# Optimization experiments

Measured on AMD Instinct MI355X. Metric: run time of the kernel, lower is better.

Reference implementation:

```python
import jax, jax.numpy as jnp
import numpy as np

N = 100000
IN_CH = 128
HID = 128
H = HID // 2  # per-sign half width = 64
E = 1200000
L = 3  # num_layers


def _mean_agg(x, src, dst, n):
    # mean of x[src] scattered to dst (source_to_target message passing)
    s = jax.ops.segment_sum(x[src], dst, num_segments=n)
    cnt = jax.ops.segment_sum(jnp.ones(src.shape[0], x.dtype), dst, num_segments=n)
    return s / jnp.maximum(cnt, 1.0)[:, None]


def setup_inputs() -> dict:
    key = jax.random.key(0)
    ks = jax.random.split(key, 16)
    sc = 0.05
    inp = {
        "x": jax.random.normal(ks[0], (N, IN_CH), jnp.float32),
        "pos_edge_index": jax.random.randint(ks[1], (2, E), 0, N, jnp.int64),
        "neg_edge_index": jax.random.randint(ks[2], (2, E), 0, N, jnp.int64),
        # conv1 (first_aggr=True): per-sign Linear on aggregated + on root
        "Wp_l": jax.random.normal(ks[3], (IN_CH, H), jnp.float32) * sc,
        "Wp_r": jax.random.normal(ks[4], (IN_CH, H), jnp.float32) * sc,
        "bp": jnp.zeros((H,), jnp.float32),
        "Wn_l": jax.random.normal(ks[5], (IN_CH, H), jnp.float32) * sc,
        "Wn_r": jax.random.normal(ks[6], (IN_CH, H), jnp.float32) * sc,
        "bn": jnp.zeros((H,), jnp.float32),
        # convs (first_aggr=False), stacked over L-1 layers
        "Wl_pos": jax.random.normal(ks[7], (L - 1, 2 * H, H), jnp.float32) * sc,
        "Wr_pos": jax.random.normal(ks[8], (L - 1, H, H), jnp.float32) * sc,
        "b_pos": jnp.zeros((L - 1, H), jnp.float32),
        "Wl_neg": jax.random.normal(ks[9], (L - 1, 2 * H, H), jnp.float32) * sc,
        "Wr_neg": jax.random.normal(ks[10], (L - 1, H, H), jnp.float32) * sc,
        "b_neg": jnp.zeros((L - 1, H), jnp.float32),
    }
    return inp


def reference(x, pos_edge_index, neg_edge_index,
              Wp_l, Wp_r, bp, Wn_l, Wn_r, bn,
              Wl_pos, Wr_pos, b_pos, Wl_neg, Wr_neg, b_neg):
    n = x.shape[0]
    ps, pd = pos_edge_index[0], pos_edge_index[1]
    ns, nd = neg_edge_index[0], neg_edge_index[1]

    # ---- conv1, first_aggr=True ----
    agg_p = _mean_agg(x, ps, pd, n)   # [N, IN_CH]
    agg_n = _mean_agg(x, ns, nd, n)
    out_pos = agg_p @ Wp_l + x @ Wp_r + bp   # [N, H]
    out_neg = agg_n @ Wn_l + x @ Wn_r + bn
    z = jnp.tanh(jnp.concatenate([out_pos, out_neg], axis=1))  # [N, 2H]

    # ---- convs, first_aggr=False ----
    for l in range(Wl_pos.shape[0]):
        x_p, x_n = z[:, :H], z[:, H:]
        ap_p = _mean_agg(x_p, ps, pd, n)   # pos-agg of pos half
        an_n = _mean_agg(x_n, ns, nd, n)   # neg-agg of neg half
        ap_n = _mean_agg(x_n, ps, pd, n)   # pos-agg of neg half
        an_p = _mean_agg(x_p, ns, nd, n)   # neg-agg of pos half
        o_p = (jnp.concatenate([ap_p, an_n], axis=1) @ Wl_pos[l]
               + x_p @ Wr_pos[l] + b_pos[l])
        o_n = (jnp.concatenate([ap_n, an_p], axis=1) @ Wl_neg[l]
               + x_n @ Wr_neg[l] + b_neg[l])
        z = jnp.tanh(jnp.concatenate([o_p, o_n], axis=1))
    return z  # [N, HID]
```

## Files before the change

kernel.cpp:

```cpp
#include <hip/hip_runtime.h>
#include <math.h>

#define CH 128
#define BSHIFT 9
#define BNODES (1 << BSHIFT)
#define CHUNKE 16384

typedef __attribute__((ext_vector_type(8))) short bf16x8;
typedef __attribute__((ext_vector_type(4))) float f32x4;

__global__ __launch_bounds__(256) void hist_kernel(const int* __restrict__ pe,
                                                   const int* __restrict__ ne,
                                                   int* __restrict__ hb,
                                                   int NBr, int G, int M, int E) {
    const int g = blockIdx.x, s = blockIdx.y, t = threadIdx.x;
    const int* __restrict__ dst = (s ? ne : pe) + E;
    __shared__ int h[512];
    for (int i = t; i < NBr; i += 256) h[i] = 0;
    __syncthreads();
    const int e0 = g * CHUNKE, e1 = min(e0 + CHUNKE, E);
    for (int e = e0 + t; e < e1; e += 256) atomicAdd(&h[dst[e] >> BSHIFT], 1);
    __syncthreads();
    int* out = hb + (size_t)s * M;
    for (int b = t; b < NBr; b += 256) out[b * G + g] = h[b];
}

__global__ __launch_bounds__(1024) void hscan_kernel(int* __restrict__ hb, int M) {
    const int s = blockIdx.y, t = threadIdx.x;
    int* H = hb + (size_t)s * M;
    const int K = (M + 1023) >> 10;
    const int i0 = t * K, i1 = min(i0 + K, M);
    int sum = 0;
    for (int i = i0; i < i1; ++i) sum += H[i];
    __shared__ int sh[1024];
    sh[t] = sum;
    __syncthreads();
    for (int off = 1; off < 1024; off <<= 1) {
        int v = (t >= off) ? sh[t - off] : 0;
        __syncthreads();
        sh[t] += v;
        __syncthreads();
    }
    int run = sh[t] - sum;
    for (int i = i0; i < i1; ++i) { int v = H[i]; H[i] = run; run += v; }
}

__global__ __launch_bounds__(256) void scatter_kernel(const int* __restrict__ pe,
                                                      const int* __restrict__ ne,
                                                      const int* __restrict__ hb,
                                                      int* __restrict__ tmp,
                                                      int NBr, int G, int M, int E) {
    const int g = blockIdx.x, s = blockIdx.y, t = threadIdx.x;
    const int* __restrict__ ed = s ? ne : pe;
    const int* off = hb + (size_t)s * M;
    __shared__ int cur[512];
    for (int b = t; b < NBr; b += 256) cur[b] = off[b * G + g];
    __syncthreads();
    int* out = tmp + (size_t)s * E;
    const int e0 = g * CHUNKE, e1 = min(e0 + CHUNKE, E);
    for (int e = e0 + t; e < e1; e += 256) {
        const int src = ed[e], d = ed[E + e];
        const int p = atomicAdd(&cur[d >> BSHIFT], 1);
        out[p] = (src << BSHIFT) | (d & (BNODES - 1));
    }
}

__global__ __launch_bounds__(256) void bucket_kernel(const int* __restrict__ tmp,
                                                     const int* __restrict__ hb,
                                                     int* __restrict__ row_p,
                                                     int* __restrict__ row_n,
                                                     int* __restrict__ csr_p,
                                                     int* __restrict__ csr_n,
                                                     int NBr, int G, int M, int E, int nN) {
    const int b = blockIdx.x, s = blockIdx.y, t = threadIdx.x;
    const int* off = hb + (size_t)s * M;
    const int lo = off[b * G];
    const int hi = (b + 1 < NBr) ? off[(b + 1) * G] : E;
    const int base = b << BSHIFT;
    const int nloc = min(BNODES, nN - base);
    const int* __restrict__ in = tmp + (size_t)s * E;
    int* __restrict__ row = s ? row_n : row_p;
    int* __restrict__ csr = s ? csr_n : csr_p;
    __shared__ int cnt[BNODES];
    __shared__ int psum[256];
    for (int i = t; i < BNODES; i += 256) cnt[i] = 0;
    __syncthreads();
    for (int e = lo + t; e < hi; e += 256) atomicAdd(&cnt[in[e] & (BNODES - 1)], 1);
    __syncthreads();
    const int c0 = cnt[2 * t], c1 = cnt[2 * t + 1];
    const int ps = c0 + c1;
    psum[t] = ps;
    __syncthreads();
    for (int o = 1; o < 256; o <<= 1) {
        int v = (t >= o) ? psum[t - o] : 0;
        __syncthreads();
        psum[t] += v;
        __syncthreads();
    }
    const int ex = psum[t] - ps;
    cnt[2 * t]     = lo + ex;
    cnt[2 * t + 1] = lo + ex + c0;
    if (2 * t < nloc)     row[base + 2 * t] = lo + ex;
    if (2 * t + 1 < nloc) row[base + 2 * t + 1] = lo + ex + c0;
    if (b == NBr - 1 && t == 0) row[nN] = E;
    __syncthreads();
    for (int e = lo + t; e < hi; e += 256) {
        const int v = in[e];
        const int p = atomicAdd(&cnt[v & (BNODES - 1)], 1);
        csr[p] = v >> BSHIFT;
    }
}

__device__ __forceinline__ float fast_tanh(float x) {
    float e = __expf(2.0f * x);
    return 1.0f - 2.0f * __builtin_amdgcn_rcpf(e + 1.0f);
}

__device__ __forceinline__ unsigned short f2bf(float f) {
    unsigned u = __float_as_uint(f);
    u += 0x7fffu + ((u >> 16) & 1u);
    return (unsigned short)(u >> 16);
}

__device__ __forceinline__ float bf_lo(unsigned v) { return __uint_as_float(v << 16); }
__device__ __forceinline__ float bf_hi(unsigned v) { return __uint_as_float(v & 0xffff0000u); }

template <bool FP32IN>
__global__ __launch_bounds__(256) void agg_kernel(
    const void* __restrict__ featv,
    unsigned* __restrict__ aggp, unsigned* __restrict__ aggn,
    const int* __restrict__ row_p, const int* __restrict__ csr_p,
    const int* __restrict__ row_n, const int* __restrict__ csr_n, int nN) {
    const int t = threadIdx.x;
    const int wave = __builtin_amdgcn_readfirstlane(t >> 6);
    const int lane = t & 63;
    const int node = blockIdx.x * 2 + (wave >> 1);
    const int sign = wave & 1;
    if (node >= nN) return;
    const int* __restrict__ rowp = sign ? row_n : row_p;
    const int* __restrict__ csr = sign ? csr_n : csr_p;
    unsigned* __restrict__ out = sign ? aggn : aggp;
    const int s0 = rowp[node], s1 = rowp[node + 1];
    float ax = 0.f, ay = 0.f;
    int e = s0;
    if (FP32IN) {
        const float* feat = (const float*)featv;
        for (; e + 7 < s1; e += 8) {
            const int a0 = csr[e], a1 = csr[e+1], a2 = csr[e+2], a3 = csr[e+3];
            const int a4 = csr[e+4], a5 = csr[e+5], a6 = csr[e+6], a7 = csr[e+7];
            const float2 v0 = ((const float2*)(feat + (size_t)a0 * CH))[lane];
            const float2 v1 = ((const float2*)(feat + (size_t)a1 * CH))[lane];
            const float2 v2 = ((const float2*)(feat + (size_t)a2 * CH))[lane];
            const float2 v3 = ((const float2*)(feat + (size_t)a3 * CH))[lane];
            const float2 v4 = ((const float2*)(feat + (size_t)a4 * CH))[lane];
            const float2 v5 = ((const float2*)(feat + (size_t)a5 * CH))[lane];
            const float2 v6 = ((const float2*)(feat + (size_t)a6 * CH))[lane];
            const float2 v7 = ((const float2*)(feat + (size_t)a7 * CH))[lane];
            ax += ((v0.x + v1.x) + (v2.x + v3.x)) + ((v4.x + v5.x) + (v6.x + v7.x));
            ay += ((v0.y + v1.y) + (v2.y + v3.y)) + ((v4.y + v5.y) + (v6.y + v7.y));
        }
        for (; e + 1 < s1; e += 2) {
            const int a0 = csr[e], a1 = csr[e + 1];
            const float2 v0 = ((const float2*)(feat + (size_t)a0 * CH))[lane];
            const float2 v1 = ((const float2*)(feat + (size_t)a1 * CH))[lane];
            ax += v0.x + v1.x;
            ay += v0.y + v1.y;
        }
        if (e < s1) {
            const float2 v0 = ((const float2*)(feat + (size_t)csr[e] * CH))[lane];
            ax += v0.x; ay += v0.y;
        }
    } else {
        const unsigned short* feat = (const unsigned short*)featv;
        for (; e + 7 < s1; e += 8) {
            const int a0 = csr[e], a1 = csr[e+1], a2 = csr[e+2], a3 = csr[e+3];
            const int a4 = csr[e+4], a5 = csr[e+5], a6 = csr[e+6], a7 = csr[e+7];
            const unsigned v0 = ((const unsigned*)(feat + (size_t)a0 * CH))[lane];
            const unsigned v1 = ((const unsigned*)(feat + (size_t)a1 * CH))[lane];
            const unsigned v2 = ((const unsigned*)(feat + (size_t)a2 * CH))[lane];
            const unsigned v3 = ((const unsigned*)(feat + (size_t)a3 * CH))[lane];
            const unsigned v4 = ((const unsigned*)(feat + (size_t)a4 * CH))[lane];
            const unsigned v5 = ((const unsigned*)(feat + (size_t)a5 * CH))[lane];
            const unsigned v6 = ((const unsigned*)(feat + (size_t)a6 * CH))[lane];
            const unsigned v7 = ((const unsigned*)(feat + (size_t)a7 * CH))[lane];
            ax += ((bf_lo(v0) + bf_lo(v1)) + (bf_lo(v2) + bf_lo(v3))) +
                  ((bf_lo(v4) + bf_lo(v5)) + (bf_lo(v6) + bf_lo(v7)));
            ay += ((bf_hi(v0) + bf_hi(v1)) + (bf_hi(v2) + bf_hi(v3))) +
                  ((bf_hi(v4) + bf_hi(v5)) + (bf_hi(v6) + bf_hi(v7)));
        }
        for (; e + 1 < s1; e += 2) {
            const unsigned v0 = ((const unsigned*)(feat + (size_t)csr[e] * CH))[lane];
            const unsigned v1 = ((const unsigned*)(feat + (size_t)csr[e + 1] * CH))[lane];
            ax += bf_lo(v0) + bf_lo(v1);
            ay += bf_hi(v0) + bf_hi(v1);
        }
        if (e < s1) {
            const unsigned v0 = ((const unsigned*)(feat + (size_t)csr[e] * CH))[lane];
            ax += bf_lo(v0); ay += bf_hi(v0);
        }
    }
    const int d = s1 - s0;
    const float inv = 1.0f / (float)(d > 1 ? d : 1);
    ax *= inv; ay *= inv;
    out[(size_t)node * 64 + lane] = (unsigned)f2bf(ax) | ((unsigned)f2bf(ay) << 16);
}

__global__ __launch_bounds__(64) void wpack_kernel(
    const float* __restrict__ Wp_l, const float* __restrict__ Wp_r,
    const float* __restrict__ Wn_l, const float* __restrict__ Wn_r,
    const float* __restrict__ Wl_pos, const float* __restrict__ Wr_pos,
    const float* __restrict__ Wl_neg, const float* __restrict__ Wr_neg,
    unsigned short* __restrict__ Wpk) {
    const int b = blockIdx.x;
    const int L = b / 96;
    const int rem = b % 96;
    const int ks = rem / 8, nt = rem % 8;
    const int lane = threadIdx.x;
    const int kb = ks * 32 + (lane >> 4) * 8;
    const int n = nt * 16 + (lane & 15);
    unsigned short v[8];
#pragma unroll
    for (int j = 0; j < 8; ++j) {
        const int k = kb + j;
        float w = 0.f;
        if (L == 0) {
            if (k < 128)      w = (n < 64) ? Wp_l[k * 64 + n] : 0.f;
            else if (k < 256) w = (n < 64) ? 0.f : Wn_l[(k - 128) * 64 + (n - 64)];
            else              w = (n < 64) ? Wp_r[(k - 256) * 64 + n]
                                           : Wn_r[(k - 256) * 64 + (n - 64)];
        } else {
            const float* WLp = Wl_pos + (size_t)(L - 1) * 128 * 64;
            const float* WLn = Wl_neg + (size_t)(L - 1) * 128 * 64;
            const float* WRp = Wr_pos + (size_t)(L - 1) * 64 * 64;
            const float* WRn = Wr_neg + (size_t)(L - 1) * 64 * 64;
            if (k < 64)       w = (n < 64) ? WLp[k * 64 + n] : 0.f;
            else if (k < 128) w = (n < 64) ? 0.f : WLn[(k - 64) * 64 + (n - 64)];
            else if (k < 192) w = (n < 64) ? 0.f : WLn[(64 + k - 128) * 64 + (n - 64)];
            else if (k < 256) w = (n < 64) ? WLp[(64 + k - 192) * 64 + n] : 0.f;
            else if (k < 320) w = (n < 64) ? WRp[(k - 256) * 64 + n] : 0.f;
            else              w = (n < 64) ? 0.f : WRn[(k - 320) * 64 + (n - 64)];
        }
        v[j] = f2bf(w);
    }
    unsigned short* dst = Wpk + (size_t)b * 512 + lane * 8;
#pragma unroll
    for (int j = 0; j < 8; ++j) dst[j] = v[j];
}

__global__ void bcat_kernel(const float* __restrict__ bp, const float* __restrict__ bn,
                            const float* __restrict__ b_pos, const float* __restrict__ b_neg,
                            float* __restrict__ bcat) {
    int t = threadIdx.x;
    int L = t >> 7, n = t & 127;
    float v;
    if (L == 0) v = (n < 64) ? bp[n] : bn[n - 64];
    else        v = (n < 64) ? b_pos[(L - 1) * 64 + n] : b_neg[(L - 1) * 64 + (n - 64)];
    bcat[t] = v;
}

template <bool XF32, bool OUTF32>
__global__ __launch_bounds__(256) void gemm_kernel(
    const unsigned short* __restrict__ aggp, const unsigned short* __restrict__ aggn,
    const void* __restrict__ featv, const unsigned short* __restrict__ Wpk,
    const float* __restrict__ bcat, void* __restrict__ outv, int nN) {
    const int t = threadIdx.x;
    const int wave = __builtin_amdgcn_readfirstlane(t >> 6);
    const int lane = t & 63;
    const int r0 = blockIdx.x * 64 + wave * 16;
    int rowA = r0 + (lane & 15);
    if (rowA >= nN) rowA = nN - 1;
    const int koff = (lane >> 4) * 8;

    f32x4 acc[8];
#pragma unroll
    for (int i = 0; i < 8; ++i) acc[i] = (f32x4){0.f, 0.f, 0.f, 0.f};

#pragma unroll
    for (int ks = 0; ks < 12; ++ks) {
        const int kcol = (ks & 3) * 32 + koff;
        bf16x8 a;
        if (ks < 4) {
            a = *(const bf16x8*)(aggp + (size_t)rowA * CH + kcol);
        } else if (ks < 8) {
            a = *(const bf16x8*)(aggn + (size_t)rowA * CH + kcol);
        } else if (XF32) {
            const float* p = (const float*)featv + (size_t)rowA * CH + kcol;
            const float4 u0 = *(const float4*)(p);
            const float4 u1 = *(const float4*)(p + 4);
            union { bf16x8 v; unsigned short u[8]; } au;
            au.u[0] = f2bf(u0.x); au.u[1] = f2bf(u0.y);
            au.u[2] = f2bf(u0.z); au.u[3] = f2bf(u0.w);
            au.u[4] = f2bf(u1.x); au.u[5] = f2bf(u1.y);
            au.u[6] = f2bf(u1.z); au.u[7] = f2bf(u1.w);
            a = au.v;
        } else {
            a = *(const bf16x8*)((const unsigned short*)featv + (size_t)rowA * CH + kcol);
        }
        const unsigned short* wb = Wpk + (size_t)(ks * 8) * 512 + lane * 8;
#pragma unroll
        for (int nt = 0; nt < 8; ++nt) {
            const bf16x8 bfr = *(const bf16x8*)(wb + nt * 512);
            acc[nt] = __builtin_amdgcn_mfma_f32_16x16x32_bf16(a, bfr, acc[nt], 0, 0, 0);
        }
    }

    const int col0 = lane & 15;
    const int rq = (lane >> 4) * 4;
#pragma unroll
    for (int nt = 0; nt < 8; ++nt) {
        const int col = nt * 16 + col0;
        const float bias = bcat[col];
#pragma unroll
        for (int r = 0; r < 4; ++r) {
            const int row = r0 + rq + r;
            if (row < nN) {
                const float v = fast_tanh(acc[nt][r] + bias);
                if (OUTF32) ((float*)outv)[(size_t)row * CH + col] = v;
                else ((unsigned short*)outv)[(size_t)row * CH + col] = f2bf(v);
            }
        }
    }
}

extern "C" void kernel_launch(void* const* d_in, const int* in_sizes, int n_in,
                              void* d_out, int out_size, void* d_ws, size_t ws_size,
                              hipStream_t stream) {
    const float* x      = (const float*)d_in[0];
    const int*   pe     = (const int*)d_in[1];
    const int*   ne     = (const int*)d_in[2];
    const float* Wp_l   = (const float*)d_in[3];
    const float* Wp_r   = (const float*)d_in[4];
    const float* bp     = (const float*)d_in[5];
    const float* Wn_l   = (const float*)d_in[6];
    const float* Wn_r   = (const float*)d_in[7];
    const float* bn     = (const float*)d_in[8];
    const float* Wl_pos = (const float*)d_in[9];
    const float* Wr_pos = (const float*)d_in[10];
    const float* b_pos  = (const float*)d_in[11];
    const float* Wl_neg = (const float*)d_in[12];
    const float* Wr_neg = (const float*)d_in[13];
    const float* b_neg  = (const float*)d_in[14];

    const int E = in_sizes[1] / 2;
    const int n = in_sizes[0] / CH;

    const int NBr = (n + BNODES - 1) >> BSHIFT;
    const int G   = (E + CHUNKE - 1) / CHUNKE;
    const int M   = NBr * G;

    unsigned short* A    = (unsigned short*)d_ws;
    unsigned short* B    = A + (size_t)n * CH;
    unsigned short* C    = B + (size_t)n * CH;
    unsigned short* Wpk  = C + (size_t)n * CH;
    float* bcat  = (float*)(Wpk + 147456);
    int* row_p   = (int*)(bcat + 384);
    int* row_n   = row_p + n + 1;
    int* csr_p   = row_n + n + 1;
    int* csr_n   = csr_p + E;
    int* hb      = csr_n + E;
    int* tmp     = (int*)C;

    hist_kernel<<<dim3(G, 2), 256, 0, stream>>>(pe, ne, hb, NBr, G, M, E);
    wpack_kernel<<<288, 64, 0, stream>>>(Wp_l, Wp_r, Wn_l, Wn_r,
                                         Wl_pos, Wr_pos, Wl_neg, Wr_neg, Wpk);
    bcat_kernel<<<1, 384, 0, stream>>>(bp, bn, b_pos, b_neg, bcat);
    hscan_kernel<<<dim3(1, 2), 1024, 0, stream>>>(hb, M);
    scatter_kernel<<<dim3(G, 2), 256, 0, stream>>>(pe, ne, hb, tmp, NBr, G, M, E);
    bucket_kernel<<<dim3(NBr, 2), 256, 0, stream>>>(tmp, hb, row_p, row_n,
                                                    csr_p, csr_n, NBr, G, M, E, n);

    const dim3 agrid((n + 1) / 2), ablock(256);
    const dim3 ggrid((n + 63) / 64), gblock(256);

    agg_kernel<true><<<agrid, ablock, 0, stream>>>(
        x, (unsigned*)A, (unsigned*)B, row_p, csr_p, row_n, csr_n, n);
    gemm_kernel<true, false><<<ggrid, gblock, 0, stream>>>(
        A, B, x, Wpk, bcat, A, n);
    agg_kernel<false><<<agrid, ablock, 0, stream>>>(
        A, (unsigned*)B, (unsigned*)C, row_p, csr_p, row_n, csr_n, n);
    gemm_kernel<false, false><<<ggrid, gblock, 0, stream>>>(
        B, C, A, Wpk + 96 * 512, bcat + 128, B, n);
    agg_kernel<false><<<agrid, ablock, 0, stream>>>(
        B, (unsigned*)A, (unsigned*)C, row_p, csr_p, row_n, csr_n, n);
    gemm_kernel<false, true><<<ggrid, gblock, 0, stream>>>(
        A, C, B, Wpk + 2 * 96 * 512, bcat + 256, d_out, n);
}
```

Baseline: 694.7 us.

## Pre-convert input features to bf16 and merge pos/neg gathers per wave

Adds a conversion kernel that casts x to bf16 once, so the first-layer aggregation gathers half-width rows and the first GEMM no longer converts on the fly. The aggregation kernel now processes both edge signs for a node in one wave, interleaving the two gather streams for more memory-level parallelism. The cost is an extra conversion pass over x and first-layer sums taken from bf16-rounded inputs.

```diff
diff --git a/kernel.cpp b/kernel.cpp
--- a/kernel.cpp
+++ b/kernel.cpp
@@ -125,84 +125,84 @@
 __device__ __forceinline__ float bf_lo(unsigned v) { return __uint_as_float(v << 16); }
 __device__ __forceinline__ float bf_hi(unsigned v) { return __uint_as_float(v & 0xffff0000u); }
 
-template <bool FP32IN>
+__global__ __launch_bounds__(256) void cvt_kernel(const float* __restrict__ x,
+                                                  unsigned short* __restrict__ xb,
+                                                  int total8) {
+    const int i = blockIdx.x * 256 + threadIdx.x;
+    if (i >= total8) return;
+    const float4 u0 = ((const float4*)x)[2 * i];
+    const float4 u1 = ((const float4*)x)[2 * i + 1];
+    union { bf16x8 v; unsigned short u[8]; } o;
+    o.u[0] = f2bf(u0.x); o.u[1] = f2bf(u0.y); o.u[2] = f2bf(u0.z); o.u[3] = f2bf(u0.w);
+    o.u[4] = f2bf(u1.x); o.u[5] = f2bf(u1.y); o.u[6] = f2bf(u1.z); o.u[7] = f2bf(u1.w);
+    ((bf16x8*)xb)[i] = o.v;
+}
+
+#define G8(csr, e, ax, ay) { \
+    const int a0 = csr[e], a1 = csr[e+1], a2 = csr[e+2], a3 = csr[e+3]; \
+    const int a4 = csr[e+4], a5 = csr[e+5], a6 = csr[e+6], a7 = csr[e+7]; \
+    const unsigned w0 = ((const unsigned*)(feat + (size_t)a0 * CH))[lane]; \
+    const unsigned w1 = ((const unsigned*)(feat + (size_t)a1 * CH))[lane]; \
+    const unsigned w2 = ((const unsigned*)(feat + (size_t)a2 * CH))[lane]; \
+    const unsigned w3 = ((const unsigned*)(feat + (size_t)a3 * CH))[lane]; \
+    const unsigned w4 = ((const unsigned*)(feat + (size_t)a4 * CH))[lane]; \
+    const unsigned w5 = ((const unsigned*)(feat + (size_t)a5 * CH))[lane]; \
+    const unsigned w6 = ((const unsigned*)(feat + (size_t)a6 * CH))[lane]; \
+    const unsigned w7 = ((const unsigned*)(feat + (size_t)a7 * CH))[lane]; \
+    ax += ((bf_lo(w0) + bf_lo(w1)) + (bf_lo(w2) + bf_lo(w3))) + \
+          ((bf_lo(w4) + bf_lo(w5)) + (bf_lo(w6) + bf_lo(w7))); \
+    ay += ((bf_hi(w0) + bf_hi(w1)) + (bf_hi(w2) + bf_hi(w3))) + \
+          ((bf_hi(w4) + bf_hi(w5)) + (bf_hi(w6) + bf_hi(w7))); }
+
+#define G4(csr, e, ax, ay) { \
+    const int a0 = csr[e], a1 = csr[e+1], a2 = csr[e+2], a3 = csr[e+3]; \
+    const unsigned w0 = ((const unsigned*)(feat + (size_t)a0 * CH))[lane]; \
+    const unsigned w1 = ((const unsigned*)(feat + (size_t)a1 * CH))[lane]; \
+    const unsigned w2 = ((const unsigned*)(feat + (size_t)a2 * CH))[lane]; \
+    const unsigned w3 = ((const unsigned*)(feat + (size_t)a3 * CH))[lane]; \
+    ax += (bf_lo(w0) + bf_lo(w1)) + (bf_lo(w2) + bf_lo(w3)); \
+    ay += (bf_hi(w0) + bf_hi(w1)) + (bf_hi(w2) + bf_hi(w3)); }
+
+#define G1(csr, e, ax, ay) { \
+    const unsigned w0 = ((const unsigned*)(feat + (size_t)csr[e] * CH))[lane]; \
+    ax += bf_lo(w0); ay += bf_hi(w0); }
+
 __global__ __launch_bounds__(256) void agg_kernel(
-    const void* __restrict__ featv,
+    const unsigned short* __restrict__ feat,
     unsigned* __restrict__ aggp, unsigned* __restrict__ aggn,
     const int* __restrict__ row_p, const int* __restrict__ csr_p,
     const int* __restrict__ row_n, const int* __restrict__ csr_n, int nN) {
     const int t = threadIdx.x;
-    const int wave = __builtin_amdgcn_readfirstlane(t >> 6);
+    const int wave = t >> 6;
     const int lane = t & 63;
-    const int node = blockIdx.x * 2 + (wave >> 1);
-    const int sign = wave & 1;
+    const int node = blockIdx.x * 4 + wave;
     if (node >= nN) return;
-    const int* __restrict__ rowp = sign ? row_n : row_p;
-    const int* __restrict__ csr = sign ? csr_n : csr_p;
-    unsigned* __restrict__ out = sign ? aggn : aggp;
-    const int s0 = rowp[node], s1 = rowp[node + 1];
-    float ax = 0.f, ay = 0.f;
-    int e = s0;
-    if (FP32IN) {
-        const float* feat = (const float*)featv;
-        for (; e + 7 < s1; e += 8) {
-            const int a0 = csr[e], a1 = csr[e+1], a2 = csr[e+2], a3 = csr[e+3];
-            const int a4 = csr[e+4], a5 = csr[e+5], a6 = csr[e+6], a7 = csr[e+7];
-            const float2 v0 = ((const float2*)(feat + (size_t)a0 * CH))[lane];
-            const float2 v1 = ((const float2*)(feat + (size_t)a1 * CH))[lane];
-            const float2 v2 = ((const float2*)(feat + (size_t)a2 * CH))[lane];
-            const float2 v3 = ((const float2*)(feat + (size_t)a3 * CH))[lane];
-            const float2 v4 = ((const float2*)(feat + (size_t)a4 * CH))[lane];
-            const float2 v5 = ((const float2*)(feat + (size_t)a5 * CH))[lane];
-            const float2 v6 = ((const float2*)(feat + (size_t)a6 * CH))[lane];
-            const float2 v7 = ((const float2*)(feat + (size_t)a7 * CH))[lane];
-            ax += ((v0.x + v1.x) + (v2.x + v3.x)) + ((v4.x + v5.x) + (v6.x + v7.x));
-            ay += ((v0.y + v1.y) + (v2.y + v3.y)) + ((v4.y + v5.y) + (v6.y + v7.y));
-        }
-        for (; e + 1 < s1; e += 2) {
-            const int a0 = csr[e], a1 = csr[e + 1];
-            const float2 v0 = ((const float2*)(feat + (size_t)a0 * CH))[lane];
-            const float2 v1 = ((const float2*)(feat + (size_t)a1 * CH))[lane];
-            ax += v0.x + v1.x;
-            ay += v0.y + v1.y;
-        }
-        if (e < s1) {
-            const float2 v0 = ((const float2*)(feat + (size_t)csr[e] * CH))[lane];
-            ax += v0.x; ay += v0.y;
-        }
-    } else {
-        const unsigned short* feat = (const unsigned short*)featv;
-        for (; e + 7 < s1; e += 8) {
-            const int a0 = csr[e], a1 = csr[e+1], a2 = csr[e+2], a3 = csr[e+3];
-            const int a4 = csr[e+4], a5 = csr[e+5], a6 = csr[e+6], a7 = csr[e+7];
-            const unsigned v0 = ((const unsigned*)(feat + (size_t)a0 * CH))[lane];
-            const unsigned v1 = ((const unsigned*)(feat + (size_t)a1 * CH))[lane];
-            const unsigned v2 = ((const unsigned*)(feat + (size_t)a2 * CH))[lane];
-            const unsigned v3 = ((const unsigned*)(feat + (size_t)a3 * CH))[lane];
-            const unsigned v4 = ((const unsigned*)(feat + (size_t)a4 * CH))[lane];
-            const unsigned v5 = ((const unsigned*)(feat + (size_t)a5 * CH))[lane];
-            const unsigned v6 = ((const unsigned*)(feat + (size_t)a6 * CH))[lane];
-            const unsigned v7 = ((const unsigned*)(feat + (size_t)a7 * CH))[lane];
-            ax += ((bf_lo(v0) + bf_lo(v1)) + (bf_lo(v2) + bf_lo(v3))) +
-                  ((bf_lo(v4) + bf_lo(v5)) + (bf_lo(v6) + bf_lo(v7)));
-            ay += ((bf_hi(v0) + bf_hi(v1)) + (bf_hi(v2) + bf_hi(v3))) +
-                  ((bf_hi(v4) + bf_hi(v5)) + (bf_hi(v6) + bf_hi(v7)));
-        }
-        for (; e + 1 < s1; e += 2) {
-            const unsigned v0 = ((const unsigned*)(feat + (size_t)csr[e] * CH))[lane];
-            const unsigned v1 = ((const unsigned*)(feat + (size_t)csr[e + 1] * CH))[lane];
-            ax += bf_lo(v0) + bf_lo(v1);
-            ay += bf_hi(v0) + bf_hi(v1);
-        }
-        if (e < s1) {
-            const unsigned v0 = ((const unsigned*)(feat + (size_t)csr[e] * CH))[lane];
-            ax += bf_lo(v0); ay += bf_hi(v0);
-        }
-    }
-    const int d = s1 - s0;
-    const float inv = 1.0f / (float)(d > 1 ? d : 1);
-    ax *= inv; ay *= inv;
-    out[(size_t)node * 64 + lane] = (unsigned)f2bf(ax) | ((unsigned)f2bf(ay) << 16);
+    int ep = row_p[node]; const int e1p = row_p[node + 1];
+    int en = row_n[node]; const int e1n = row_n[node + 1];
+    const int degp = e1p - ep;
+    const int degn = e1n - en;
+    float axp = 0.f, ayp = 0.f, axn = 0.f, ayn = 0.f;
+    while (ep + 8 <= e1p && en + 8 <= e1n) {
+        G8(csr_p, ep, axp, ayp);
+        G8(csr_n, en, axn, ayn);
+        ep += 8; en += 8;
+    }
+    while (ep + 4 <= e1p && en + 4 <= e1n) {
+        G4(csr_p, ep, axp, ayp);
+        G4(csr_n, en, axn, ayn);
+        ep += 4; en += 4;
+    }
+    for (; ep + 7 < e1p; ep += 8) G8(csr_p, ep, axp, ayp);
+    if (ep + 3 < e1p) { G4(csr_p, ep, axp, ayp); ep += 4; }
+    for (; ep < e1p; ++ep) G1(csr_p, ep, axp, ayp);
+    for (; en + 7 < e1n; en += 8) G8(csr_n, en, axn, ayn);
+    if (en + 3 < e1n) { G4(csr_n, en, axn, ayn); en += 4; }
+    for (; en < e1n; ++en) G1(csr_n, en, axn, ayn);
+
+    const float invp = 1.0f / (float)(degp > 1 ? degp : 1);
+    const float invn = 1.0f / (float)(degn > 1 ? degn : 1);
+    aggp[(size_t)node * 64 + lane] = (unsigned)f2bf(axp * invp) | ((unsigned)f2bf(ayp * invp) << 16);
+    aggn[(size_t)node * 64 + lane] = (unsigned)f2bf(axn * invn) | ((unsigned)f2bf(ayn * invn) << 16);
 }
 
 __global__ __launch_bounds__(64) void wpack_kernel(
@@ -258,10 +258,10 @@
     bcat[t] = v;
 }
 
-template <bool XF32, bool OUTF32>
+template <bool OUTF32>
 __global__ __launch_bounds__(256) void gemm_kernel(
     const unsigned short* __restrict__ aggp, const unsigned short* __restrict__ aggn,
-    const void* __restrict__ featv, const unsigned short* __restrict__ Wpk,
+    const unsigned short* __restrict__ feat, const unsigned short* __restrict__ Wpk,
     const float* __restrict__ bcat, void* __restrict__ outv, int nN) {
     const int t = threadIdx.x;
     const int wave = __builtin_amdgcn_readfirstlane(t >> 6);
@@ -278,24 +278,8 @@
 #pragma unroll
     for (int ks = 0; ks < 12; ++ks) {
         const int kcol = (ks & 3) * 32 + koff;
-        bf16x8 a;
-        if (ks < 4) {
-            a = *(const bf16x8*)(aggp + (size_t)rowA * CH + kcol);
-        } else if (ks < 8) {
-            a = *(const bf16x8*)(aggn + (size_t)rowA * CH + kcol);
-        } else if (XF32) {
-            const float* p = (const float*)featv + (size_t)rowA * CH + kcol;
-            const float4 u0 = *(const float4*)(p);
-            const float4 u1 = *(const float4*)(p + 4);
-            union { bf16x8 v; unsigned short u[8]; } au;
-            au.u[0] = f2bf(u0.x); au.u[1] = f2bf(u0.y);
-            au.u[2] = f2bf(u0.z); au.u[3] = f2bf(u0.w);
-            au.u[4] = f2bf(u1.x); au.u[5] = f2bf(u1.y);
-            au.u[6] = f2bf(u1.z); au.u[7] = f2bf(u1.w);
-            a = au.v;
-        } else {
-            a = *(const bf16x8*)((const unsigned short*)featv + (size_t)rowA * CH + kcol);
-        }
+        const unsigned short* ap = (ks < 4) ? aggp : (ks < 8) ? aggn : feat;
+        const bf16x8 a = *(const bf16x8*)(ap + (size_t)rowA * CH + kcol);
         const unsigned short* wb = Wpk + (size_t)(ks * 8) * 512 + lane * 8;
 #pragma unroll
         for (int nt = 0; nt < 8; ++nt) {
@@ -359,6 +343,7 @@
     int* csr_n   = csr_p + E;
     int* hb      = csr_n + E;
     int* tmp     = (int*)C;
+    unsigned short* xb = C;
 
     hist_kernel<<<dim3(G, 2), 256, 0, stream>>>(pe, ne, hb, NBr, G, M, E);
     wpack_kernel<<<288, 64, 0, stream>>>(Wp_l, Wp_r, Wn_l, Wn_r,
@@ -368,20 +353,22 @@
     scatter_kernel<<<dim3(G, 2), 256, 0, stream>>>(pe, ne, hb, tmp, NBr, G, M, E);
     bucket_kernel<<<dim3(NBr, 2), 256, 0, stream>>>(tmp, hb, row_p, row_n,
                                                     csr_p, csr_n, NBr, G, M, E, n);
-
-    const dim3 agrid((n + 1) / 2), ablock(256);
+    const int total8 = n * CH / 8;
+    cvt_kernel<<<(total8 + 255) / 256, 256, 0, stream>>>(x, xb, total8);
+
+    const dim3 agrid((n + 3) / 4), ablock(256);
     const dim3 ggrid((n + 63) / 64), gblock(256);
 
-    agg_kernel<true><<<agrid, ablock, 0, stream>>>(
-        x, (unsigned*)A, (unsigned*)B, row_p, csr_p, row_n, csr_n, n);
-    gemm_kernel<true, false><<<ggrid, gblock, 0, stream>>>(
-        A, B, x, Wpk, bcat, A, n);
-    agg_kernel<false><<<agrid, ablock, 0, stream>>>(
+    agg_kernel<<<agrid, ablock, 0, stream>>>(
+        xb, (unsigned*)A, (unsigned*)B, row_p, csr_p, row_n, csr_n, n);
+    gemm_kernel<false><<<ggrid, gblock, 0, stream>>>(
+        A, B, xb, Wpk, bcat, A, n);
+    agg_kernel<<<agrid, ablock, 0, stream>>>(
         A, (unsigned*)B, (unsigned*)C, row_p, csr_p, row_n, csr_n, n);
-    gemm_kernel<false, false><<<ggrid, gblock, 0, stream>>>(
+    gemm_kernel<false><<<ggrid, gblock, 0, stream>>>(
         B, C, A, Wpk + 96 * 512, bcat + 128, B, n);
-    agg_kernel<false><<<agrid, ablock, 0, stream>>>(
+    agg_kernel<<<agrid, ablock, 0, stream>>>(
         B, (unsigned*)A, (unsigned*)C, row_p, csr_p, row_n, csr_n, n);
-    gemm_kernel<false, true><<<ggrid, gblock, 0, stream>>>(
+    gemm_kernel<true><<<ggrid, gblock, 0, stream>>>(
         A, C, B, Wpk + 2 * 96 * 512, bcat + 256, d_out, n);
 }
```

Result: faster. 637.4 us (-8.2%).
